# Kernel tuning notes

Hardware: AMD Instinct MI355X
Metric: run time of the kernel (lower is better)

Reference implementation:

```python
import jax, jax.numpy as jnp
import numpy as np

B, C, T = 16, 256, 2048
K = 1024  # codes per layer
N_LAYERS = 3


def setup_inputs() -> dict:
    key = jax.random.key(0)
    kx, k0, k1, k2 = jax.random.split(key, 4)
    x = jax.random.normal(kx, (B, C, T), dtype=jnp.float32)
    scale = 1.0 / K
    emb0 = jax.random.uniform(k0, (K, C), minval=-scale, maxval=scale, dtype=jnp.float32)
    emb1 = jax.random.uniform(k1, (K, C), minval=-scale, maxval=scale, dtype=jnp.float32)
    emb2 = jax.random.uniform(k2, (K, C), minval=-scale, maxval=scale, dtype=jnp.float32)
    return {"x": x, "emb0": emb0, "emb1": emb1, "emb2": emb2}


def _vq_layer(x, emb):
    # x: [B, C, T], emb: [K, C]
    b, c, t = x.shape
    flat = jnp.transpose(x, (0, 2, 1)).reshape(-1, c)          # [B*T, C]
    # squared L2 distance to each code: ||f||^2 - 2 f.e + ||e||^2
    dist = (jnp.sum(flat * flat, axis=1, keepdims=True)
            - 2.0 * flat @ emb.T
            + jnp.sum(emb * emb, axis=1))                       # [B*T, K]
    idx = jnp.argmin(dist, axis=1)                              # [B*T]
    quant = jnp.transpose(emb[idx].reshape(b, t, c), (0, 2, 1)) # [B, C, T]
    sg = jax.lax.stop_gradient
    loss = jnp.mean((sg(quant) - x) ** 2) + jnp.mean((quant - sg(x)) ** 2)
    quantized = x + sg(quant - x)  # straight-through
    return quantized, loss


def reference(x, emb0, emb1, emb2):
    total_loss = jnp.float32(0.0)
    out = x
    for emb in (emb0, emb1, emb2):
        out, loss = _vq_layer(out, emb)
        total_loss = total_loss + loss
    return out, total_loss
```

## Files before the change

kernel.cpp:

```cpp
#include <hip/hip_runtime.h>
#include <stdint.h>

#define B_  16
#define C_  256
#define T_  2048
#define K_  1024
#define TOTAL_ELEMS 8388608

typedef short bf16x8 __attribute__((ext_vector_type(8)));
typedef float f32x4 __attribute__((ext_vector_type(4)));

__device__ __forceinline__ unsigned long long pack_key(float d, int idx) {
  unsigned u = __float_as_uint(d);
  u = (u & 0x80000000u) ? ~u : (u | 0x80000000u);
  return ((unsigned long long)u << 32) | (unsigned)idx;
}
__device__ __forceinline__ float unpack_dist(unsigned long long key) {
  unsigned du = (unsigned)(key >> 32);
  unsigned bits = (du & 0x80000000u) ? (du ^ 0x80000000u) : ~du;
  return __uint_as_float(bits);
}

__device__ __forceinline__ unsigned short f2bf_rne(float f) {
  unsigned u = __float_as_uint(f);
  unsigned r = u + 0x7FFFu + ((u >> 16) & 1u);
  return (unsigned short)(r >> 16);
}

__global__ __launch_bounds__(256) void prep_kernel(
    const float* __restrict__ e0, const float* __restrict__ e1,
    const float* __restrict__ e2, float* __restrict__ nrm,
    unsigned short* __restrict__ ebt, uint4* __restrict__ keysM_region,
    float* __restrict__ loss_accum, unsigned* __restrict__ counter) {
  int bid = blockIdx.x;
  int tid = threadIdx.x;
  if (bid < 12) {
    int i = bid * 256 + tid;
    const float* e = (i < 1024) ? e0 : (i < 2048) ? e1 : e2;
    const float* p = e + (size_t)(i & 1023) * C_;
    float s = 0.0f;
    for (int c = 0; c < C_; c += 4) {
      float4 v = *(const float4*)(p + c);
      s = fmaf(v.x, v.x, s); s = fmaf(v.y, v.y, s);
      s = fmaf(v.z, v.z, s); s = fmaf(v.w, v.w, s);
    }
    nrm[i] = s;
  } else if (bid < 268) {
    int code = (bid - 12) * 4 + (tid >> 6);
    int c = (tid & 63) * 4;
    float4 v = *(const float4*)(e0 + (size_t)code * C_ + c);
    unsigned lo = (unsigned)f2bf_rne(v.x) | ((unsigned)f2bf_rne(v.y) << 16);
    unsigned hi = (unsigned)f2bf_rne(v.z) | ((unsigned)f2bf_rne(v.w) << 16);
    int kk = c >> 5, lg = (c >> 3) & 3, j = c & 7;
    *(uint2*)(ebt + ((size_t)(kk * 1024 + code) * 4 + lg) * 8 + j) = make_uint2(lo, hi);
  } else {
    int i = (bid - 268) * 256 + tid;
    keysM_region[i] = make_uint4(0xFFFFFFFFu, 0xFFFFFFFFu, 0xFFFFFFFFu, 0xFFFFFFFFu);
    if (bid == 268 && tid == 0) { *loss_accum = 0.0f; *counter = 0u; }
  }
}

__global__ __launch_bounds__(256) void map_tile_kernel(
    const float* __restrict__ e0, const float* __restrict__ e1,
    const float* __restrict__ e2, const float* __restrict__ nrm,
    unsigned long long* __restrict__ keysM) {
  __shared__ float As[16][68];
  __shared__ float Bs[16][68];
  int bid = blockIdx.x;
  int m = bid >> 8;
  int tb = bid & 255;
  int ar0 = (tb >> 4) << 6;
  int br0 = (tb & 15) << 6;
  const float* Ap = m ? e1 : e0;
  const float* Bp = m ? e2 : e1;
  const float* nB = nrm + (m + 1) * 1024;

  int tid = threadIdx.x;
  int ty = tid >> 4, tx = tid & 15;
  int srow = tid >> 2;
  int skp  = (tid & 3) << 2;

  float acc[4][4];
#pragma unroll
  for (int i = 0; i < 4; i++)
#pragma unroll
    for (int j = 0; j < 4; j++) acc[i][j] = 0.0f;

  const float* gA = Ap + (size_t)(ar0 + srow) * C_ + skp;
  const float* gB = Bp + (size_t)(br0 + srow) * C_ + skp;

  for (int kk = 0; kk < C_; kk += 16) {
    float4 av = *(const float4*)(gA + kk);
    float4 bv = *(const float4*)(gB + kk);
    __syncthreads();
    As[skp + 0][srow] = av.x; As[skp + 1][srow] = av.y;
    As[skp + 2][srow] = av.z; As[skp + 3][srow] = av.w;
    Bs[skp + 0][srow] = bv.x; Bs[skp + 1][srow] = bv.y;
    Bs[skp + 2][srow] = bv.z; Bs[skp + 3][srow] = bv.w;
    __syncthreads();
#pragma unroll
    for (int k = 0; k < 16; k++) {
      float4 a4 = *(const float4*)&As[k][ty * 4];
      float4 b4 = *(const float4*)&Bs[k][tx * 4];
      float aa[4] = {a4.x, a4.y, a4.z, a4.w};
      float bb[4] = {b4.x, b4.y, b4.z, b4.w};
#pragma unroll
      for (int i = 0; i < 4; i++)
#pragma unroll
        for (int j = 0; j < 4; j++)
          acc[i][j] = fmaf(aa[i], bb[j], acc[i][j]);
    }
  }

  float nv[4];
#pragma unroll
  for (int j = 0; j < 4; j++) nv[j] = nB[br0 + tx * 4 + j];

#pragma unroll
  for (int i = 0; i < 4; i++) {
    unsigned long long best = 0xFFFFFFFFFFFFFFFFULL;
#pragma unroll
    for (int j = 0; j < 4; j++) {
      int code = br0 + tx * 4 + j;
      float s = nv[j] - 2.0f * acc[i][j];
      unsigned long long key = pack_key(s, code);
      if (key < best) best = key;
    }
#pragma unroll
    for (int off = 1; off < 16; off <<= 1) {
      unsigned long long o = __shfl_xor(best, off, 64);
      if (o < best) best = o;
    }
    if (tx == 0)
      atomicMin(&keysM[m * 1024 + ar0 + ty * 4 + i], best);
  }
}

__global__ __launch_bounds__(256, 2) void l0_fused_kernel(
    const float* __restrict__ x, const unsigned short* __restrict__ ebt,
    const float* __restrict__ e0n, unsigned long long* __restrict__ keys,
    float* __restrict__ loss_accum) {
  __shared__ __align__(16) char Abuf[32768];
  __shared__ unsigned long long kred[64][2];
  __shared__ float red[4];

  int tid = threadIdx.x;
  int l = tid & 63, w = tid >> 6;
  int lr = l & 15, lg = l >> 4;
  int wr = w >> 1, wc = w & 1;
  int row0 = blockIdx.x << 6;

  {
    int bb = blockIdx.x >> 5;
    int t0 = (blockIdx.x & 31) << 6;
    const float* xb = x + (size_t)bb * (C_ * T_) + t0 + l;
    float sumsq = 0.0f;
#pragma unroll
    for (int i = 0; i < 8; i++) {
      int c0 = w * 64 + i * 8;
      float v[8];
#pragma unroll
      for (int u = 0; u < 8; u++) {
        v[u] = __builtin_nontemporal_load(xb + (size_t)(c0 + u) * T_);
        sumsq = fmaf(v[u], v[u], sumsq);
      }
      unsigned pk[4];
#pragma unroll
      for (int j = 0; j < 4; j++)
        pk[j] = (unsigned)f2bf_rne(v[2 * j]) | ((unsigned)f2bf_rne(v[2 * j + 1]) << 16);
      int cc = w * 8 + i;
      *(uint4*)(Abuf + ((size_t)cc * 64 + l) * 16) =
          make_uint4(pk[0], pk[1], pk[2], pk[3]);
    }
    for (int off = 32; off > 0; off >>= 1) sumsq += __shfl_down(sumsq, off, 64);
    if (l == 0) red[w] = sumsq;
  }
  __syncthreads();
  if (tid == 0)
    atomicAdd(loss_accum, red[0] + red[1] + red[2] + red[3]);

  const unsigned short* pB = ebt + (size_t)(wc * 64 + lr) * 32 + lg * 8;

#define LOADB(s, p_, kk_) do {                                               \
    const unsigned short* q_ = pB + (size_t)(kk_) * 32768 + (size_t)(p_) * 4096; \
    s##0 = *(const bf16x8*)(q_);                                             \
    s##1 = *(const bf16x8*)(q_ + 512);                                       \
    s##2 = *(const bf16x8*)(q_ + 1024);                                      \
    s##3 = *(const bf16x8*)(q_ + 1536);                                      \
  } while (0)

#define DOKK(kk_, s) do {                                                    \
    const char* ab_ = Abuf + (size_t)((kk_) * 4 + lg) * 1024 +               \
                      (wr * 32 + lr) * 16;                                   \
    bf16x8 a0_ = *(const bf16x8*)(ab_);                                      \
    bf16x8 a1_ = *(const bf16x8*)(ab_ + 256);                                \
    acc[0][0] = __builtin_amdgcn_mfma_f32_16x16x32_bf16(a0_, s##0, acc[0][0], 0, 0, 0); \
    acc[1][0] = __builtin_amdgcn_mfma_f32_16x16x32_bf16(a1_, s##0, acc[1][0], 0, 0, 0); \
    acc[0][1] = __builtin_amdgcn_mfma_f32_16x16x32_bf16(a0_, s##1, acc[0][1], 0, 0, 0); \
    acc[1][1] = __builtin_amdgcn_mfma_f32_16x16x32_bf16(a1_, s##1, acc[1][1], 0, 0, 0); \
    acc[0][2] = __builtin_amdgcn_mfma_f32_16x16x32_bf16(a0_, s##2, acc[0][2], 0, 0, 0); \
    acc[1][2] = __builtin_amdgcn_mfma_f32_16x16x32_bf16(a1_, s##2, acc[1][2], 0, 0, 0); \
    acc[0][3] = __builtin_amdgcn_mfma_f32_16x16x32_bf16(a0_, s##3, acc[0][3], 0, 0, 0); \
    acc[1][3] = __builtin_amdgcn_mfma_f32_16x16x32_bf16(a1_, s##3, acc[1][3], 0, 0, 0); \
  } while (0)

  f32x4 acc[2][4];
  float bestv[2][4];
  int   bestm[2][4];
#pragma unroll
  for (int mi = 0; mi < 2; mi++)
#pragma unroll
    for (int r = 0; r < 4; r++) { bestv[mi][r] = -1e30f; bestm[mi][r] = 0; }

  bf16x8 bA0, bA1, bA2, bA3, bB0, bB1, bB2, bB3;
  LOADB(bA, 0, 0);

  for (int p = 0; p < 8; p++) {
#pragma unroll
    for (int ni = 0; ni < 4; ni++) {
      float iv = -0.5f * e0n[p * 128 + wc * 64 + ni * 16 + lr];
      f32x4 ivv = {iv, iv, iv, iv};
      acc[0][ni] = ivv;
      acc[1][ni] = ivv;
    }
#pragma unroll
    for (int kh = 0; kh < 4; kh++) {
      const int kk0 = 2 * kh, kk1 = 2 * kh + 1;
      LOADB(bB, p, kk1);
      DOKK(kk0, bA);
      if (kk1 < 7)    { LOADB(bA, p, kk1 + 1); }
      else if (p < 7) { LOADB(bA, p + 1, 0); }
      DOKK(kk1, bB);
    }
#pragma unroll
    for (int mi = 0; mi < 2; mi++)
#pragma unroll
      for (int r = 0; r < 4; r++)
#pragma unroll
        for (int ni = 0; ni < 4; ni++) {
          float v = acc[mi][ni][r];
          if (v > bestv[mi][r]) { bestv[mi][r] = v; bestm[mi][r] = p * 4 + ni; }
        }
  }
#undef LOADB
#undef DOKK

#pragma unroll
  for (int mi = 0; mi < 2; mi++)
#pragma unroll
    for (int r = 0; r < 4; r++) {
      float sdist = -2.0f * bestv[mi][r];
      int m = bestm[mi][r];
      int code = ((m >> 2) << 7) | (wc << 6) | ((m & 3) << 4) | lr;
      unsigned long long key = pack_key(sdist, code);
#pragma unroll
      for (int off = 1; off < 16; off <<= 1) {
        unsigned long long o = __shfl_xor(key, off, 64);
        if (o < key) key = o;
      }
      if (lr == 0) kred[wr * 32 + mi * 16 + lg * 4 + r][wc] = key;
    }
  __syncthreads();
  if (tid < 64) {
    unsigned long long b0 = kred[tid][0], b1 = kred[tid][1];
    keys[row0 + tid] = b0 < b1 ? b0 : b1;
  }
}

__global__ __launch_bounds__(256) void finish_kernel(
    const float* __restrict__ emb2,
    const unsigned long long* __restrict__ keys,
    const unsigned long long* __restrict__ keysM,
    const float* __restrict__ nrm,
    float* __restrict__ out, float* __restrict__ loss_accum,
    unsigned* __restrict__ counter) {
  __shared__ int code2_l[64];
  __shared__ float rloss[64];
  int tid = threadIdx.x;
  int b  = blockIdx.x >> 5;
  int t0 = (blockIdx.x & 31) << 6;
  int tt = tid & 63, w = tid >> 6;

  if (w == 0) {
    unsigned long long key0 = keys[(size_t)b * T_ + t0 + tt];
    int idx0 = (int)(key0 & 0xFFFFFFFFULL);
    float s0 = unpack_dist(key0);
    unsigned long long k1 = keysM[idx0];
    int c1 = (int)(k1 & 0xFFFFFFFFULL);
    unsigned long long k2 = keysM[1024 + c1];
    code2_l[tt] = (int)(k2 & 0xFFFFFFFFULL);
    rloss[tt] = s0 + nrm[idx0] + unpack_dist(k1) + nrm[1024 + c1] + unpack_dist(k2);
  }
  __syncthreads();

  float* ob = out + ((size_t)b << 19);
  int code2 = code2_l[tt];
  const float* e2row = emb2 + (size_t)code2 * C_;
  for (int c4 = w * 64; c4 < w * 64 + 64; c4 += 4) {
    float4 ev = *(const float4*)(e2row + c4);
    float evv[4] = {ev.x, ev.y, ev.z, ev.w};
#pragma unroll
    for (int u = 0; u < 4; u++)
      __builtin_nontemporal_store(evv[u], ob + (size_t)(c4 + u) * T_ + t0 + tt);
  }
  if (w == 0) {
    float tot = rloss[tt];
    for (int off = 32; off > 0; off >>= 1)
      tot += __shfl_down(tot, off, 64);
    if (tt == 0) atomicAdd(loss_accum, tot);
  }
  if (tid == 0) {
    __threadfence();
    unsigned old = atomicAdd(counter, 1u);
    if (old == 511u) {
      float L = atomicAdd(loss_accum, 0.0f);
      out[TOTAL_ELEMS] = 2.0f * L / 8388608.0f;
    }
  }
}

extern "C" void kernel_launch(void* const* d_in, const int* in_sizes, int n_in,
                              void* d_out, int out_size, void* d_ws, size_t ws_size,
                              hipStream_t stream) {
  const float* x  = (const float*)d_in[0];
  const float* e0 = (const float*)d_in[1];
  const float* e1 = (const float*)d_in[2];
  const float* e2 = (const float*)d_in[3];
  float* out = (float*)d_out;
  char* ws = (char*)d_ws;

  unsigned long long* keys  = (unsigned long long*)ws;
  unsigned long long* keysM = (unsigned long long*)(ws + 262144);
  float* nrm  = (float*)(ws + 278528);
  float* loss_accum = (float*)(ws + 290816);
  unsigned* counter = (unsigned*)(ws + 290820);
  unsigned short* ebt = (unsigned short*)(ws + 294912);

  prep_kernel<<<272, 256, 0, stream>>>(e0, e1, e2, nrm, ebt, (uint4*)keysM,
                                       loss_accum, counter);
  l0_fused_kernel<<<512, 256, 0, stream>>>(x, ebt, nrm, keys, loss_accum);
  map_tile_kernel<<<512, 256, 0, stream>>>(e0, e1, e2, nrm, keysM);
  finish_kernel<<<512, 256, 0, stream>>>(e2, keys, keysM, nrm, out, loss_accum, counter);
}
```

Before: 109.4 us.

## Split layer-0 codebook search across four blocks per row tile with atomicMin merge

The layer-0 distance kernel now launches four times as many blocks. Each block handles 64 rows against a quarter of the codebook (256 codes), with each wave covering 64 codes and all 64 rows, instead of one block sweeping all 1024 codes in 8 passes. Partial argmins are combined with atomicMin on the keys array, so prep now initialises keys and keysM to all-ones as one contiguous region. This aims to fill more CUs and shorten the per-block serial chain, but each x tile is now loaded and converted four times, and the nontemporal hint on those loads is dropped.

Result: no change. 108.0 us (-1.3%).

```diff
diff --git a/kernel.cpp b/kernel.cpp
--- a/kernel.cpp
+++ b/kernel.cpp
@@ -30,7 +30,7 @@
 __global__ __launch_bounds__(256) void prep_kernel(
     const float* __restrict__ e0, const float* __restrict__ e1,
     const float* __restrict__ e2, float* __restrict__ nrm,
-    unsigned short* __restrict__ ebt, uint4* __restrict__ keysM_region,
+    unsigned short* __restrict__ ebt, uint4* __restrict__ keys_region,
     float* __restrict__ loss_accum, unsigned* __restrict__ counter) {
   int bid = blockIdx.x;
   int tid = threadIdx.x;
@@ -55,7 +55,7 @@
     *(uint2*)(ebt + ((size_t)(kk * 1024 + code) * 4 + lg) * 8 + j) = make_uint2(lo, hi);
   } else {
     int i = (bid - 268) * 256 + tid;
-    keysM_region[i] = make_uint4(0xFFFFFFFFu, 0xFFFFFFFFu, 0xFFFFFFFFu, 0xFFFFFFFFu);
+    keys_region[i] = make_uint4(0xFFFFFFFFu, 0xFFFFFFFFu, 0xFFFFFFFFu, 0xFFFFFFFFu);
     if (bid == 268 && tid == 0) { *loss_accum = 0.0f; *counter = 0u; }
   }
 }
@@ -141,48 +141,51 @@
     const float* __restrict__ e0n, unsigned long long* __restrict__ keys,
     float* __restrict__ loss_accum) {
   __shared__ __align__(16) char Abuf[32768];
-  __shared__ unsigned long long kred[64][2];
+  __shared__ unsigned long long kred[64][4];
   __shared__ float red[4];
 
   int tid = threadIdx.x;
   int l = tid & 63, w = tid >> 6;
   int lr = l & 15, lg = l >> 4;
-  int wr = w >> 1, wc = w & 1;
-  int row0 = blockIdx.x << 6;
+  int q  = blockIdx.x >> 9;
+  int mb = blockIdx.x & 511;
+  int row0 = mb << 6;
 
   {
-    int bb = blockIdx.x >> 5;
-    int t0 = (blockIdx.x & 31) << 6;
-    const float* xb = x + (size_t)bb * (C_ * T_) + t0 + l;
+    int row = tid & 63;
+    int cg  = tid >> 6;
+    int bb  = mb >> 5;
+    int t0  = (mb & 31) << 6;
+    const float* xb = x + (size_t)bb * (C_ * T_) + t0 + row;
     float sumsq = 0.0f;
 #pragma unroll
     for (int i = 0; i < 8; i++) {
-      int c0 = w * 64 + i * 8;
+      int c0 = cg * 64 + i * 8;
       float v[8];
 #pragma unroll
       for (int u = 0; u < 8; u++) {
-        v[u] = __builtin_nontemporal_load(xb + (size_t)(c0 + u) * T_);
+        v[u] = xb[(size_t)(c0 + u) * T_];
         sumsq = fmaf(v[u], v[u], sumsq);
       }
       unsigned pk[4];
 #pragma unroll
       for (int j = 0; j < 4; j++)
         pk[j] = (unsigned)f2bf_rne(v[2 * j]) | ((unsigned)f2bf_rne(v[2 * j + 1]) << 16);
-      int cc = w * 8 + i;
-      *(uint4*)(Abuf + ((size_t)cc * 64 + l) * 16) =
+      int cc = c0 >> 3;
+      *(uint4*)(Abuf + ((size_t)cc * 64 + row) * 16) =
           make_uint4(pk[0], pk[1], pk[2], pk[3]);
     }
     for (int off = 32; off > 0; off >>= 1) sumsq += __shfl_down(sumsq, off, 64);
     if (l == 0) red[w] = sumsq;
   }
   __syncthreads();
-  if (tid == 0)
+  if (q == 0 && tid == 0)
     atomicAdd(loss_accum, red[0] + red[1] + red[2] + red[3]);
 
-  const unsigned short* pB = ebt + (size_t)(wc * 64 + lr) * 32 + lg * 8;
-
-#define LOADB(s, p_, kk_) do {                                               \
-    const unsigned short* q_ = pB + (size_t)(kk_) * 32768 + (size_t)(p_) * 4096; \
+  const unsigned short* pB = ebt + ((size_t)((q << 8) + w * 64 + lr) * 4 + lg) * 8;
+
+#define LOADB(s, kk_) do {                                                   \
+    const unsigned short* q_ = pB + (size_t)(kk_) * 32768;                   \
     s##0 = *(const bf16x8*)(q_);                                             \
     s##1 = *(const bf16x8*)(q_ + 512);                                       \
     s##2 = *(const bf16x8*)(q_ + 1024);                                      \
@@ -190,80 +193,77 @@
   } while (0)
 
 #define DOKK(kk_, s) do {                                                    \
-    const char* ab_ = Abuf + (size_t)((kk_) * 4 + lg) * 1024 +               \
-                      (wr * 32 + lr) * 16;                                   \
+    const char* ab_ = Abuf + (size_t)(((kk_) * 4 + lg) * 64 + lr) * 16;      \
     bf16x8 a0_ = *(const bf16x8*)(ab_);                                      \
     bf16x8 a1_ = *(const bf16x8*)(ab_ + 256);                                \
+    bf16x8 a2_ = *(const bf16x8*)(ab_ + 512);                                \
+    bf16x8 a3_ = *(const bf16x8*)(ab_ + 768);                                \
     acc[0][0] = __builtin_amdgcn_mfma_f32_16x16x32_bf16(a0_, s##0, acc[0][0], 0, 0, 0); \
     acc[1][0] = __builtin_amdgcn_mfma_f32_16x16x32_bf16(a1_, s##0, acc[1][0], 0, 0, 0); \
+    acc[2][0] = __builtin_amdgcn_mfma_f32_16x16x32_bf16(a2_, s##0, acc[2][0], 0, 0, 0); \
+    acc[3][0] = __builtin_amdgcn_mfma_f32_16x16x32_bf16(a3_, s##0, acc[3][0], 0, 0, 0); \
     acc[0][1] = __builtin_amdgcn_mfma_f32_16x16x32_bf16(a0_, s##1, acc[0][1], 0, 0, 0); \
     acc[1][1] = __builtin_amdgcn_mfma_f32_16x16x32_bf16(a1_, s##1, acc[1][1], 0, 0, 0); \
+    acc[2][1] = __builtin_amdgcn_mfma_f32_16x16x32_bf16(a2_, s##1, acc[2][1], 0, 0, 0); \
+    acc[3][1] = __builtin_amdgcn_mfma_f32_16x16x32_bf16(a3_, s##1, acc[3][1], 0, 0, 0); \
     acc[0][2] = __builtin_amdgcn_mfma_f32_16x16x32_bf16(a0_, s##2, acc[0][2], 0, 0, 0); \
     acc[1][2] = __builtin_amdgcn_mfma_f32_16x16x32_bf16(a1_, s##2, acc[1][2], 0, 0, 0); \
+    acc[2][2] = __builtin_amdgcn_mfma_f32_16x16x32_bf16(a2_, s##2, acc[2][2], 0, 0, 0); \
+    acc[3][2] = __builtin_amdgcn_mfma_f32_16x16x32_bf16(a3_, s##2, acc[3][2], 0, 0, 0); \
     acc[0][3] = __builtin_amdgcn_mfma_f32_16x16x32_bf16(a0_, s##3, acc[0][3], 0, 0, 0); \
     acc[1][3] = __builtin_amdgcn_mfma_f32_16x16x32_bf16(a1_, s##3, acc[1][3], 0, 0, 0); \
+    acc[2][3] = __builtin_amdgcn_mfma_f32_16x16x32_bf16(a2_, s##3, acc[2][3], 0, 0, 0); \
+    acc[3][3] = __builtin_amdgcn_mfma_f32_16x16x32_bf16(a3_, s##3, acc[3][3], 0, 0, 0); \
   } while (0)
 
-  f32x4 acc[2][4];
-  float bestv[2][4];
-  int   bestm[2][4];
-#pragma unroll
-  for (int mi = 0; mi < 2; mi++)
-#pragma unroll
-    for (int r = 0; r < 4; r++) { bestv[mi][r] = -1e30f; bestm[mi][r] = 0; }
+  f32x4 acc[4][4];
+#pragma unroll
+  for (int ni = 0; ni < 4; ni++) {
+    float iv = -0.5f * e0n[(q << 8) + w * 64 + ni * 16 + lr];
+    f32x4 ivv = {iv, iv, iv, iv};
+#pragma unroll
+    for (int mi = 0; mi < 4; mi++) acc[mi][ni] = ivv;
+  }
 
   bf16x8 bA0, bA1, bA2, bA3, bB0, bB1, bB2, bB3;
-  LOADB(bA, 0, 0);
-
-  for (int p = 0; p < 8; p++) {
-#pragma unroll
-    for (int ni = 0; ni < 4; ni++) {
-      float iv = -0.5f * e0n[p * 128 + wc * 64 + ni * 16 + lr];
-      f32x4 ivv = {iv, iv, iv, iv};
-      acc[0][ni] = ivv;
-      acc[1][ni] = ivv;
-    }
-#pragma unroll
-    for (int kh = 0; kh < 4; kh++) {
-      const int kk0 = 2 * kh, kk1 = 2 * kh + 1;
-      LOADB(bB, p, kk1);
-      DOKK(kk0, bA);
-      if (kk1 < 7)    { LOADB(bA, p, kk1 + 1); }
-      else if (p < 7) { LOADB(bA, p + 1, 0); }
-      DOKK(kk1, bB);
-    }
-#pragma unroll
-    for (int mi = 0; mi < 2; mi++)
-#pragma unroll
-      for (int r = 0; r < 4; r++)
-#pragma unroll
-        for (int ni = 0; ni < 4; ni++) {
-          float v = acc[mi][ni][r];
-          if (v > bestv[mi][r]) { bestv[mi][r] = v; bestm[mi][r] = p * 4 + ni; }
-        }
-  }
+  LOADB(bA, 0);
+  LOADB(bB, 1); DOKK(0, bA);
+  LOADB(bA, 2); DOKK(1, bB);
+  LOADB(bB, 3); DOKK(2, bA);
+  LOADB(bA, 4); DOKK(3, bB);
+  LOADB(bB, 5); DOKK(4, bA);
+  LOADB(bA, 6); DOKK(5, bB);
+  LOADB(bB, 7); DOKK(6, bA);
+  DOKK(7, bB);
 #undef LOADB
 #undef DOKK
 
 #pragma unroll
-  for (int mi = 0; mi < 2; mi++)
+  for (int mi = 0; mi < 4; mi++) {
 #pragma unroll
     for (int r = 0; r < 4; r++) {
-      float sdist = -2.0f * bestv[mi][r];
-      int m = bestm[mi][r];
-      int code = ((m >> 2) << 7) | (wc << 6) | ((m & 3) << 4) | lr;
-      unsigned long long key = pack_key(sdist, code);
+      unsigned long long best = 0xFFFFFFFFFFFFFFFFULL;
+#pragma unroll
+      for (int ni = 0; ni < 4; ni++) {
+        int code = (q << 8) | (w << 6) | (ni << 4) | lr;
+        unsigned long long key = pack_key(-2.0f * acc[mi][ni][r], code);
+        if (key < best) best = key;
+      }
 #pragma unroll
       for (int off = 1; off < 16; off <<= 1) {
-        unsigned long long o = __shfl_xor(key, off, 64);
-        if (o < key) key = o;
+        unsigned long long o = __shfl_xor(best, off, 64);
+        if (o < best) best = o;
       }
-      if (lr == 0) kred[wr * 32 + mi * 16 + lg * 4 + r][wc] = key;
-    }
+      if (lr == 0) kred[mi * 16 + lg * 4 + r][w] = best;
+    }
+  }
   __syncthreads();
   if (tid < 64) {
     unsigned long long b0 = kred[tid][0], b1 = kred[tid][1];
-    keys[row0 + tid] = b0 < b1 ? b0 : b1;
+    unsigned long long b2 = kred[tid][2], b3 = kred[tid][3];
+    if (b1 < b0) b0 = b1;
+    if (b3 < b2) b2 = b3;
+    atomicMin(&keys[row0 + tid], b0 < b2 ? b0 : b2);
   }
 }
 
@@ -336,9 +336,9 @@
   unsigned* counter = (unsigned*)(ws + 290820);
   unsigned short* ebt = (unsigned short*)(ws + 294912);
 
-  prep_kernel<<<272, 256, 0, stream>>>(e0, e1, e2, nrm, ebt, (uint4*)keysM,
+  prep_kernel<<<336, 256, 0, stream>>>(e0, e1, e2, nrm, ebt, (uint4*)ws,
                                        loss_accum, counter);
-  l0_fused_kernel<<<512, 256, 0, stream>>>(x, ebt, nrm, keys, loss_accum);
+  l0_fused_kernel<<<2048, 256, 0, stream>>>(x, ebt, nrm, keys, loss_accum);
   map_tile_kernel<<<512, 256, 0, stream>>>(e0, e1, e2, nrm, keysM);
   finish_kernel<<<512, 256, 0, stream>>>(e2, keys, keysM, nrm, out, loss_accum, counter);
 }
```
